# Optimization experiments

Measured on AMD Instinct MI355X. Metric: run time of the kernel, lower is better.

The kernel has to match this reference:

```python
import jax, jax.numpy as jnp
import numpy as np

NODE_NUM = 100000
LAYER_NUM = 4
EMB = 128
FEAT = 256
BATCH = 4096
NEIGH = 32
EPS = 1e-12  # F.normalize default eps


def setup_inputs() -> dict:
    key = jax.random.key(0)
    ks = jax.random.split(key, 10)
    std = 1.0 / np.sqrt(EMB)
    return {
        "layers": jax.random.randint(ks[0], (BATCH,), 0, LAYER_NUM),
        "node_i": jax.random.randint(ks[1], (BATCH,), 0, NODE_NUM),
        "neighs_i": jax.random.randint(ks[2], (BATCH, LAYER_NUM, NEIGH), 0, NODE_NUM),
        "features": jax.random.normal(ks[3], (NODE_NUM, FEAT), dtype=jnp.float32),
        "layer_embs": jax.random.uniform(ks[4], (NODE_NUM, LAYER_NUM, EMB), dtype=jnp.float32, minval=-1.0, maxval=1.0),
        "neigh_emb_trans": jax.random.normal(ks[5], (LAYER_NUM, FEAT, EMB), dtype=jnp.float32) * std,
        "trans_weights": jax.random.normal(ks[6], (EMB, EMB), dtype=jnp.float32) * std,
        "trans_weights_s1": jax.random.normal(ks[7], (EMB, EMB), dtype=jnp.float32) * std,
        "trans_weights_s2": jax.random.normal(ks[8], (EMB, 1), dtype=jnp.float32) * std,
    }


def reference(layers, node_i, neighs_i, features, layer_embs, neigh_emb_trans,
              trans_weights, trans_weights_s1, trans_weights_s2):
    # Gather neighbor features: [B, L, J, F]
    feats_n = features[neighs_i]
    # Per-layer linear transform == diagonal of torch's 'bijk,akm->bijam' over (i,a):
    # [B, L, J, M]
    h = jnp.einsum('bljf,lfm->bljm', feats_n, neigh_emb_trans)
    # Sum over neighbors -> [B, L, M]
    h = h.sum(axis=2)
    # Attention over layers: tanh(h @ Ws1) @ Ws2 -> [B, L]
    scores = jnp.squeeze(jnp.tanh(h @ trans_weights_s1) @ trans_weights_s2, axis=-1)
    att = jax.nn.softmax(scores, axis=1)  # [B, L]
    # Attention-weighted layer aggregation -> [B, M]
    agg = jnp.einsum('bl,blm->bm', att, h)
    node_embed = agg @ trans_weights  # [B, M]
    final = node_embed + layer_embs[node_i, layers]  # residual with per-(node,layer) emb
    # F.normalize(dim=1): x / max(||x||_2, eps)
    norm = jnp.linalg.norm(final, axis=1, keepdims=True)
    return final / jnp.maximum(norm, EPS)
```

## Files before the change

kernel.cpp:

```cpp
#include <hip/hip_runtime.h>
#include <hip/hip_bf16.h>
#include <math.h>

#define BATCH 4096
#define LNUM  4
#define NEIGH 32
#define FEAT  256
#define EMB   128

#define B_TILE 4
#define ROWS   (B_TILE * LNUM)

__global__ __launch_bounds__(256, 4) void fused_liamne(
    const int* __restrict__ layers, const int* __restrict__ node_i,
    const int* __restrict__ neighs, const float* __restrict__ features,
    const float* __restrict__ layer_embs, const float* __restrict__ W,
    const float* __restrict__ Wt, const float* __restrict__ Ws1,
    const float* __restrict__ Ws2, float* __restrict__ out) {
  __shared__ float sS[ROWS][FEAT];
  __shared__ float sH[ROWS][EMB];
  __shared__ float sc[ROWS];

  int b0 = blockIdx.x * B_TILE;
  int tid = threadIdx.x;
  int w = tid >> 6;
  int lane = tid & 63;

  {
    int nIdx[LNUM];
#pragma unroll
    for (int l = 0; l < LNUM; ++l) {
      const int* nbr = neighs + ((size_t)(b0 + w) * LNUM + l) * NEIGH;
      nIdx[l] = nbr[lane & 31];
    }
    const float4* f4 = (const float4*)features;
    float4 acc[LNUM];
#pragma unroll
    for (int l = 0; l < LNUM; ++l) acc[l] = make_float4(0.f, 0.f, 0.f, 0.f);
#pragma unroll
    for (int jj = 0; jj < 8; ++jj) {
      float4 v[LNUM][4];
#pragma unroll
      for (int l = 0; l < LNUM; ++l)
#pragma unroll
        for (int q = 0; q < 4; ++q) {
          int n = __shfl(nIdx[l], jj * 4 + q, 64);
          v[l][q] = f4[(size_t)n * (FEAT / 4) + lane];
        }
#pragma unroll
      for (int l = 0; l < LNUM; ++l)
#pragma unroll
        for (int q = 0; q < 4; ++q) {
          acc[l].x += v[l][q].x; acc[l].y += v[l][q].y;
          acc[l].z += v[l][q].z; acc[l].w += v[l][q].w;
        }
    }
#pragma unroll
    for (int l = 0; l < LNUM; ++l)
      ((float4*)sS[w * LNUM + l])[lane] = acc[l];
  }
  __syncthreads();

  {
    const float* Wl = W + (size_t)w * FEAT * EMB;
    float acc[B_TILE][2] = {};
    for (int k = 0; k < FEAT; k += 4) {
      float4 s[B_TILE];
#pragma unroll
      for (int lb = 0; lb < B_TILE; ++lb)
        s[lb] = *(const float4*)&sS[lb * LNUM + w][k];
#pragma unroll
      for (int kk = 0; kk < 4; ++kk) {
        float2 wv = *(const float2*)&Wl[(size_t)(k + kk) * EMB + lane * 2];
#pragma unroll
        for (int lb = 0; lb < B_TILE; ++lb) {
          float sv = ((const float*)&s[lb])[kk];
          acc[lb][0] += sv * wv.x;
          acc[lb][1] += sv * wv.y;
        }
      }
    }
#pragma unroll
    for (int lb = 0; lb < B_TILE; ++lb)
      *(float2*)&sH[lb * LNUM + w][lane * 2] =
          make_float2(acc[lb][0], acc[lb][1]);
  }
  __syncthreads();

  {
    float acc[4][2] = {};
    for (int k = 0; k < EMB; k += 4) {
      float4 h[4];
#pragma unroll
      for (int i = 0; i < 4; ++i)
        h[i] = *(const float4*)&sH[w * 4 + i][k];
#pragma unroll
      for (int kk = 0; kk < 4; ++kk) {
        float2 wv = *(const float2*)&Ws1[(size_t)(k + kk) * EMB + lane * 2];
#pragma unroll
        for (int i = 0; i < 4; ++i) {
          float hv = ((const float*)&h[i])[kk];
          acc[i][0] += hv * wv.x;
          acc[i][1] += hv * wv.y;
        }
      }
    }
    float2 w2 = *(const float2*)&Ws2[lane * 2];
#pragma unroll
    for (int i = 0; i < 4; ++i) {
      float p = tanhf(acc[i][0]) * w2.x + tanhf(acc[i][1]) * w2.y;
#pragma unroll
      for (int m = 1; m < 64; m <<= 1) p += __shfl_xor(p, m, 64);
      if (lane == 0) sc[w * 4 + i] = p;
    }
  }
  __syncthreads();

  float* sAgg = &sS[0][0];
  for (int i = tid; i < B_TILE * EMB; i += 256) {
    int lb = i >> 7, m = i & 127;
    float s0 = sc[lb * 4 + 0], s1 = sc[lb * 4 + 1];
    float s2 = sc[lb * 4 + 2], s3 = sc[lb * 4 + 3];
    float mx = fmaxf(fmaxf(s0, s1), fmaxf(s2, s3));
    float e0 = expf(s0 - mx), e1 = expf(s1 - mx);
    float e2 = expf(s2 - mx), e3 = expf(s3 - mx);
    float inv = 1.0f / (e0 + e1 + e2 + e3);
    float a = e0 * sH[lb * 4 + 0][m] + e1 * sH[lb * 4 + 1][m] +
              e2 * sH[lb * 4 + 2][m] + e3 * sH[lb * 4 + 3][m];
    sAgg[i] = a * inv;
  }
  __syncthreads();

  {
    float ax = 0.f, ay = 0.f;
    for (int k = 0; k < EMB; ++k) {
      float2 wv = *(const float2*)&Wt[(size_t)k * EMB + lane * 2];
      float a = sAgg[w * EMB + k];
      ax += a * wv.x;
      ay += a * wv.y;
    }
    int b = b0 + w;
    int node = node_i[b];
    int lay = layers[b];
    float2 e = *(const float2*)&layer_embs[((size_t)node * LNUM + lay) * EMB +
                                           lane * 2];
    ax += e.x;
    ay += e.y;
    float ss = ax * ax + ay * ay;
#pragma unroll
    for (int m = 1; m < 64; m <<= 1) ss += __shfl_xor(ss, m, 64);
    float inv = 1.0f / fmaxf(sqrtf(ss), 1e-12f);
    *(float2*)&out[(size_t)b * EMB + lane * 2] =
        make_float2(ax * inv, ay * inv);
  }
}

extern "C" void kernel_launch(void* const* d_in, const int* in_sizes, int n_in,
                              void* d_out, int out_size, void* d_ws,
                              size_t ws_size, hipStream_t stream) {
  const int* layers = (const int*)d_in[0];
  const int* node_i = (const int*)d_in[1];
  const int* neighs = (const int*)d_in[2];
  const float* features = (const float*)d_in[3];
  const float* layer_embs = (const float*)d_in[4];
  const float* neigh_emb_trans = (const float*)d_in[5];
  const float* trans_weights = (const float*)d_in[6];
  const float* trans_weights_s1 = (const float*)d_in[7];
  const float* trans_weights_s2 = (const float*)d_in[8];
  float* out = (float*)d_out;

  fused_liamne<<<dim3(BATCH / B_TILE), 256, 0, stream>>>(
      layers, node_i, neighs, features, layer_embs, neigh_emb_trans,
      trans_weights, trans_weights_s1, trans_weights_s2, out);
}
```

Measured before the change: 396.6 us.

## Double block to 512 threads, splitting gather and matmul work across eight waves

Raises the thread count per block from 256 to 512. The neighbor gather is split so each wave handles two layers of one batch row. Every matmul stage now splits output columns into two 64-wide halves, one per wave group. Cross-half score and norm partial sums go through shared memory, which costs an extra barrier. The goal is more in-flight gather loads and more latency hiding per block, at the cost of narrower per-thread work and a higher launch-bound occupancy target that may limit registers.

```diff
diff --git a/kernel.cpp b/kernel.cpp
--- a/kernel.cpp
+++ b/kernel.cpp
@@ -10,8 +10,9 @@
 
 #define B_TILE 4
 #define ROWS   (B_TILE * LNUM)
+#define THREADS 512
 
-__global__ __launch_bounds__(256, 4) void fused_liamne(
+__global__ __launch_bounds__(THREADS, 8) void fused_liamne(
     const int* __restrict__ layers, const int* __restrict__ node_i,
     const int* __restrict__ neighs, const float* __restrict__ features,
     const float* __restrict__ layer_embs, const float* __restrict__ W,
@@ -19,7 +20,8 @@
     const float* __restrict__ Ws2, float* __restrict__ out) {
   __shared__ float sS[ROWS][FEAT];
   __shared__ float sH[ROWS][EMB];
-  __shared__ float sc[ROWS];
+  __shared__ float sc2[2][ROWS];
+  __shared__ float sNrm[2][B_TILE];
 
   int b0 = blockIdx.x * B_TILE;
   int tid = threadIdx.x;
@@ -27,28 +29,30 @@
   int lane = tid & 63;
 
   {
-    int nIdx[LNUM];
+    int bi = w >> 1;
+    int l0 = (w & 1) * 2;
+    int nIdx[2];
 #pragma unroll
-    for (int l = 0; l < LNUM; ++l) {
-      const int* nbr = neighs + ((size_t)(b0 + w) * LNUM + l) * NEIGH;
+    for (int l = 0; l < 2; ++l) {
+      const int* nbr = neighs + ((size_t)(b0 + bi) * LNUM + l0 + l) * NEIGH;
       nIdx[l] = nbr[lane & 31];
     }
     const float4* f4 = (const float4*)features;
-    float4 acc[LNUM];
+    float4 acc[2];
 #pragma unroll
-    for (int l = 0; l < LNUM; ++l) acc[l] = make_float4(0.f, 0.f, 0.f, 0.f);
+    for (int l = 0; l < 2; ++l) acc[l] = make_float4(0.f, 0.f, 0.f, 0.f);
 #pragma unroll
     for (int jj = 0; jj < 8; ++jj) {
-      float4 v[LNUM][4];
+      float4 v[2][4];
 #pragma unroll
-      for (int l = 0; l < LNUM; ++l)
+      for (int l = 0; l < 2; ++l)
 #pragma unroll
         for (int q = 0; q < 4; ++q) {
           int n = __shfl(nIdx[l], jj * 4 + q, 64);
           v[l][q] = f4[(size_t)n * (FEAT / 4) + lane];
         }
 #pragma unroll
-      for (int l = 0; l < LNUM; ++l)
+      for (int l = 0; l < 2; ++l)
 #pragma unroll
         for (int q = 0; q < 4; ++q) {
           acc[l].x += v[l][q].x; acc[l].y += v[l][q].y;
@@ -56,102 +60,97 @@
         }
     }
 #pragma unroll
-    for (int l = 0; l < LNUM; ++l)
-      ((float4*)sS[w * LNUM + l])[lane] = acc[l];
+    for (int l = 0; l < 2; ++l)
+      ((float4*)sS[bi * LNUM + l0 + l])[lane] = acc[l];
   }
   __syncthreads();
 
   {
-    const float* Wl = W + (size_t)w * FEAT * EMB;
-    float acc[B_TILE][2] = {};
+    int l = w & 3, mh = w >> 2;
+    const float* Wl = W + (size_t)l * FEAT * EMB + mh * 64 + lane;
+    float acc[B_TILE] = {};
     for (int k = 0; k < FEAT; k += 4) {
       float4 s[B_TILE];
 #pragma unroll
       for (int lb = 0; lb < B_TILE; ++lb)
-        s[lb] = *(const float4*)&sS[lb * LNUM + w][k];
+        s[lb] = *(const float4*)&sS[lb * LNUM + l][k];
 #pragma unroll
       for (int kk = 0; kk < 4; ++kk) {
-        float2 wv = *(const float2*)&Wl[(size_t)(k + kk) * EMB + lane * 2];
+        float wv = Wl[(size_t)(k + kk) * EMB];
 #pragma unroll
-        for (int lb = 0; lb < B_TILE; ++lb) {
-          float sv = ((const float*)&s[lb])[kk];
-          acc[lb][0] += sv * wv.x;
-          acc[lb][1] += sv * wv.y;
-        }
+        for (int lb = 0; lb < B_TILE; ++lb)
+          acc[lb] += ((const float*)&s[lb])[kk] * wv;
       }
     }
 #pragma unroll
     for (int lb = 0; lb < B_TILE; ++lb)
-      *(float2*)&sH[lb * LNUM + w][lane * 2] =
-          make_float2(acc[lb][0], acc[lb][1]);
+      sH[lb * LNUM + l][mh * 64 + lane] = acc[lb];
   }
   __syncthreads();
 
   {
-    float acc[4][2] = {};
+    int rg = w & 3, mh = w >> 2;
+    int col = mh * 64 + lane;
+    float acc[4] = {};
     for (int k = 0; k < EMB; k += 4) {
       float4 h[4];
 #pragma unroll
       for (int i = 0; i < 4; ++i)
-        h[i] = *(const float4*)&sH[w * 4 + i][k];
+        h[i] = *(const float4*)&sH[rg * 4 + i][k];
 #pragma unroll
       for (int kk = 0; kk < 4; ++kk) {
-        float2 wv = *(const float2*)&Ws1[(size_t)(k + kk) * EMB + lane * 2];
+        float wv = Ws1[(size_t)(k + kk) * EMB + col];
 #pragma unroll
-        for (int i = 0; i < 4; ++i) {
-          float hv = ((const float*)&h[i])[kk];
-          acc[i][0] += hv * wv.x;
-          acc[i][1] += hv * wv.y;
-        }
+        for (int i = 0; i < 4; ++i)
+          acc[i] += ((const float*)&h[i])[kk] * wv;
       }
     }
-    float2 w2 = *(const float2*)&Ws2[lane * 2];
+    float w2 = Ws2[col];
 #pragma unroll
     for (int i = 0; i < 4; ++i) {
-      float p = tanhf(acc[i][0]) * w2.x + tanhf(acc[i][1]) * w2.y;
+      float p = tanhf(acc[i]) * w2;
 #pragma unroll
       for (int m = 1; m < 64; m <<= 1) p += __shfl_xor(p, m, 64);
-      if (lane == 0) sc[w * 4 + i] = p;
+      if (lane == 0) sc2[mh][rg * 4 + i] = p;
     }
   }
   __syncthreads();
 
   float* sAgg = &sS[0][0];
-  for (int i = tid; i < B_TILE * EMB; i += 256) {
-    int lb = i >> 7, m = i & 127;
-    float s0 = sc[lb * 4 + 0], s1 = sc[lb * 4 + 1];
-    float s2 = sc[lb * 4 + 2], s3 = sc[lb * 4 + 3];
+  {
+    int lb = tid >> 7, m = tid & 127;
+    float s0 = sc2[0][lb * 4 + 0] + sc2[1][lb * 4 + 0];
+    float s1 = sc2[0][lb * 4 + 1] + sc2[1][lb * 4 + 1];
+    float s2 = sc2[0][lb * 4 + 2] + sc2[1][lb * 4 + 2];
+    float s3 = sc2[0][lb * 4 + 3] + sc2[1][lb * 4 + 3];
     float mx = fmaxf(fmaxf(s0, s1), fmaxf(s2, s3));
     float e0 = expf(s0 - mx), e1 = expf(s1 - mx);
     float e2 = expf(s2 - mx), e3 = expf(s3 - mx);
     float inv = 1.0f / (e0 + e1 + e2 + e3);
     float a = e0 * sH[lb * 4 + 0][m] + e1 * sH[lb * 4 + 1][m] +
               e2 * sH[lb * 4 + 2][m] + e3 * sH[lb * 4 + 3][m];
-    sAgg[i] = a * inv;
+    sAgg[tid] = a * inv;
   }
   __syncthreads();
 
   {
-    float ax = 0.f, ay = 0.f;
-    for (int k = 0; k < EMB; ++k) {
-      float2 wv = *(const float2*)&Wt[(size_t)k * EMB + lane * 2];
-      float a = sAgg[w * EMB + k];
-      ax += a * wv.x;
-      ay += a * wv.y;
-    }
-    int b = b0 + w;
+    int lb = w & 3, mh = w >> 2;
+    int col = mh * 64 + lane;
+    float ax = 0.f;
+    for (int k = 0; k < EMB; ++k)
+      ax += sAgg[lb * EMB + k] * Wt[(size_t)k * EMB + col];
+    int b = b0 + lb;
     int node = node_i[b];
     int lay = layers[b];
-    float2 e = *(const float2*)&layer_embs[((size_t)node * LNUM + lay) * EMB +
-                                           lane * 2];
-    ax += e.x;
-    ay += e.y;
-    float ss = ax * ax + ay * ay;
+    ax += layer_embs[((size_t)node * LNUM + lay) * EMB + col];
+    float ss = ax * ax;
 #pragma unroll
     for (int m = 1; m < 64; m <<= 1) ss += __shfl_xor(ss, m, 64);
-    float inv = 1.0f / fmaxf(sqrtf(ss), 1e-12f);
-    *(float2*)&out[(size_t)b * EMB + lane * 2] =
-        make_float2(ax * inv, ay * inv);
+    if (lane == 0) sNrm[mh][lb] = ss;
+    __syncthreads();
+    float tot = sNrm[0][lb] + sNrm[1][lb];
+    float inv = 1.0f / fmaxf(sqrtf(tot), 1e-12f);
+    out[(size_t)b * EMB + col] = ax * inv;
   }
 }
 
@@ -169,7 +168,7 @@
   const float* trans_weights_s2 = (const float*)d_in[8];
   float* out = (float*)d_out;
 
-  fused_liamne<<<dim3(BATCH / B_TILE), 256, 0, stream>>>(
+  fused_liamne<<<dim3(BATCH / B_TILE), THREADS, 0, stream>>>(
       layers, node_i, neighs, features, layer_embs, neigh_emb_trans,
       trans_weights, trans_weights_s1, trans_weights_s2, out);
 }
```

Result: slower. 407.7 us (+2.8%).
